# Kernel tuning notes

Hardware: AMD Instinct MI355X
Metric: run time of the kernel (lower is better)

Reference implementation:

```python
import jax, jax.numpy as jnp
import numpy as np

DIM, H, D = 2048, 16, 128
D_C, D_CQ, D_ROPE = 512, 1536, 64
B, T = 2, 2048


def _rope(t, cos, sin):
    # t: [..., T, D_ROPE]; cos/sin: [T, D_ROPE//2] broadcast over leading dims
    h = D_ROPE // 2
    t1, t2 = t[..., :h], t[..., h:]
    return jnp.concatenate([t1 * cos - t2 * sin, t2 * cos + t1 * sin], axis=-1)


def setup_inputs() -> dict:
    key = jax.random.key(0)
    ks = jax.random.split(key, 10)
    init = lambda k, shp, fan: (jax.random.normal(k, shp, jnp.float32) / np.sqrt(fan).astype(np.float32))
    x = jax.random.normal(ks[0], (B, T, DIM), jnp.float32)
    # RoPE tables for d_rope//2 = 32 rotary channels
    inv_freq = 1.0 / (10000.0 ** (np.arange(0, D_ROPE // 2, dtype=np.float32) / (D_ROPE // 2)))
    ang = np.arange(T, dtype=np.float32)[:, None] * inv_freq[None, :]
    cos = jnp.asarray(np.cos(ang), jnp.float32)
    sin = jnp.asarray(np.sin(ang), jnp.float32)
    return {
        "x": x,
        "cos": cos,
        "sin": sin,
        "w_kv": init(ks[1], (DIM, D_C), DIM),          # kv_compress
        "w_kdec": init(ks[2], (D_C, H * D), D_C),       # k_decompress
        "w_vdec": init(ks[3], (D_C, H * D), D_C),       # v_decompress
        "w_qc": init(ks[4], (DIM, D_CQ), DIM),          # q_compress
        "w_qdec": init(ks[5], (D_CQ, H * D), D_CQ),     # q_decompress
        "w_krope": init(ks[6], (DIM, D_ROPE), DIM),     # k_rope_proj
        "w_qrope": init(ks[7], (DIM, D_ROPE), DIM),     # q_rope_proj
        "w_o": init(ks[8], (H * D, DIM), H * D),        # wo
    }


def reference(x, cos, sin, w_kv, w_kdec, w_vdec, w_qc, w_qdec, w_krope, w_qrope, w_o):
    Bx, Tx, _ = x.shape
    # latent compress -> decompress
    c_kv = x @ w_kv                                       # [B,T,d_c]
    k = (c_kv @ w_kdec).reshape(Bx, Tx, H, D).transpose(0, 2, 1, 3)  # [B,H,T,D]
    v = (c_kv @ w_vdec).reshape(Bx, Tx, H, D).transpose(0, 2, 1, 3)
    c_q = x @ w_qc
    q = (c_q @ w_qdec).reshape(Bx, Tx, H, D).transpose(0, 2, 1, 3)
    # RoPE branch: head-shared projections, rotated then broadcast across heads
    k_rope = _rope(x @ w_krope, cos, sin)                 # [B,T,d_rope]
    q_rope = _rope(x @ w_qrope, cos, sin)
    rope_dim = min(D_ROPE, D)
    qr = jnp.broadcast_to(q_rope[:, None, :, :rope_dim], (Bx, H, Tx, rope_dim))
    kr = jnp.broadcast_to(k_rope[:, None, :, :rope_dim], (Bx, H, Tx, rope_dim))
    q = jnp.concatenate([q[..., :-rope_dim], qr], axis=-1)
    k = jnp.concatenate([k[..., :-rope_dim], kr], axis=-1)
    # causal SDPA, scale = 1/sqrt(head_dim)
    scores = jnp.einsum("bhtd,bhsd->bhts", q, k) / np.float32(np.sqrt(D))
    causal = jnp.tril(jnp.ones((Tx, Tx), dtype=bool))
    scores = jnp.where(causal, scores, jnp.float32(-1e30))
    attn = jax.nn.softmax(scores, axis=-1)
    out = jnp.einsum("bhts,bhsd->bhtd", attn, v)
    out = out.transpose(0, 2, 1, 3).reshape(Bx, Tx, H * D)
    return out @ w_o
```

## Files before the change

### kernel.cpp

```cpp
#include <hip/hip_runtime.h>
#include <stdint.h>
#include <math.h>

#define B_    2
#define T_    2048
#define DIM_  2048
#define H_    16
#define DC_   512
#define DCQ_  1536
#define NROWS (B_*T_)

typedef unsigned short u16;
typedef __attribute__((ext_vector_type(8))) __bf16 bf16x8;
typedef __attribute__((ext_vector_type(4))) float  f32x4;
typedef __attribute__((ext_vector_type(8))) unsigned short u16x8;
typedef __attribute__((ext_vector_type(4))) float  f4v;

__device__ __forceinline__ u16 f2bf(float f){
  unsigned u = __float_as_uint(f);
  u += 0x7FFFu + ((u >> 16) & 1u);
  return (u16)(u >> 16);
}
__device__ __forceinline__ float bf2f(u16 h){ return __uint_as_float(((unsigned)h) << 16); }

__device__ __forceinline__ unsigned cvt_pk_bf16(float lo, float hi){
  unsigned r;
  asm("v_cvt_pk_bf16_f32 %0, %1, %2" : "=v"(r) : "v"(lo), "v"(hi));
  return r;
}

__device__ __forceinline__ void gld_lds16(const void* g, void* l){
  auto gp = reinterpret_cast<__attribute__((address_space(1))) unsigned int*>(
      reinterpret_cast<uintptr_t>(g));
  auto lp = reinterpret_cast<__attribute__((address_space(3))) unsigned int*>(
      reinterpret_cast<uintptr_t>(l));
  __builtin_amdgcn_global_load_lds(gp, lp, 16, 0, 0);
}

__device__ __forceinline__ f32x4 mfma16(bf16x8 a, bf16x8 b, f32x4 c){
  return __builtin_amdgcn_mfma_f32_16x16x32_bf16(a, b, c, 0, 0, 0);
}

__device__ __forceinline__ void vmwait0(){ asm volatile("s_waitcnt vmcnt(0)" ::: "memory"); }
__device__ __forceinline__ void vmwait8(){ asm volatile("s_waitcnt vmcnt(8)" ::: "memory"); }
__device__ __forceinline__ void barr(){ asm volatile("s_barrier" ::: "memory"); }

__global__ void k_detect(const u16* cosr, int* flag, int* ticket){
  if (threadIdx.x == 0) *flag = (cosr[0] == (u16)0x3F80u) ? 1 : 0;
  if (threadIdx.x < 128) ticket[threadIdx.x] = 0;
}

struct TDesc { const void* src; u16* dst; int srcStride, dstStride, cblk, nbx, blk0; };
struct TPack { TDesc d[8]; };
#define CONVBLK 8192

__global__ void k_prep(const void* __restrict__ xsrc, u16* __restrict__ x_bf,
                       TPack p, const int* flag){
  __shared__ u16 tile[64][72];
  const int bid = blockIdx.x;
  const int tid = threadIdx.x;
  const int f = *flag;
  if (bid < CONVBLK){
    if (f) return;
    int id = bid * 256 + tid;
    f4v v = reinterpret_cast<const f4v*>(xsrc)[id];
    unsigned lo = (unsigned)f2bf(v.x) | ((unsigned)f2bf(v.y) << 16);
    unsigned hi = (unsigned)f2bf(v.z) | ((unsigned)f2bf(v.w) << 16);
    reinterpret_cast<uint2*>(x_bf)[id] = make_uint2(lo, hi);
    return;
  }
  const int tb = bid - CONVBLK;
  int i = 0;
  #pragma unroll
  for (int k = 1; k < 8; ++k) if (tb >= p.d[k].blk0) i = k;
  const void* src = p.d[i].src;
  u16* dst = p.d[i].dst;
  const int srcStride = p.d[i].srcStride, dstStride = p.d[i].dstStride;
  const int rel = tb - p.d[i].blk0;
  const int bx = rel % p.d[i].nbx, by = rel / p.d[i].nbx;
  const int r0 = by << 6, c0 = bx * p.d[i].cblk;
  #pragma unroll
  for (int it = 0; it < 2; ++it){
    int task = (it << 8) + tid;
    int r = task >> 3, c8 = (task & 7) << 3;
    if (f){
      const u16* pp = (const u16*)src + (size_t)(r0 + r) * srcStride + c0 + c8;
      u16x8 v = *reinterpret_cast<const u16x8*>(pp);
      #pragma unroll
      for (int j = 0; j < 8; ++j) tile[r][c8 + j] = v[j];
    } else {
      const float* pp = (const float*)src + (size_t)(r0 + r) * srcStride + c0 + c8;
      f4v a = reinterpret_cast<const f4v*>(pp)[0];
      f4v b = reinterpret_cast<const f4v*>(pp)[1];
      tile[r][c8+0]=f2bf(a.x); tile[r][c8+1]=f2bf(a.y); tile[r][c8+2]=f2bf(a.z); tile[r][c8+3]=f2bf(a.w);
      tile[r][c8+4]=f2bf(b.x); tile[r][c8+5]=f2bf(b.y); tile[r][c8+6]=f2bf(b.z); tile[r][c8+7]=f2bf(b.w);
    }
  }
  __syncthreads();
  #pragma unroll
  for (int it = 0; it < 2; ++it){
    int task = (it << 8) + tid;
    int rr = task >> 3, cc8 = (task & 7) << 3;
    u16x8 v;
    #pragma unroll
    for (int j = 0; j < 8; ++j) v[j] = tile[cc8 + j][rr];
    *reinterpret_cast<u16x8*>(dst + (size_t)((bx << 6) + rr) * dstStride + r0 + cc8) = v;
  }
}

__global__ __launch_bounds__(256, 2) void k_gemm(
    const u16* __restrict__ A0, int lda0, const u16* __restrict__ Bt0, int K0,
    u16* __restrict__ C0, int ldc0, float os0,
    const u16* __restrict__ A1, int lda1, const u16* __restrict__ Bt1, int K1,
    u16* __restrict__ C1, int ldc1, float os1,
    int ysplit, int swz, void* outp, const int* flag,
    const u16* __restrict__ alt0, const u16* __restrict__ alt1,
    u16* __restrict__ vt0, u16* __restrict__ vt1){
  __shared__ alignas(16) u16 lds[32768];
  const int tid = threadIdx.x;
  const int wid = tid >> 6, lane = tid & 63;
  const int wr = wid >> 1, wc = wid & 1;
  const int l16 = lane & 15, g = lane >> 4;
  int lin = blockIdx.y * 32 + blockIdx.x;
  if (swz){
    const int q8 = (gridDim.x * gridDim.y) >> 3;
    lin = (lin & 7) * q8 + (lin >> 3);
  }
  const int m0 = (lin & 31) << 7;
  int nt = lin >> 5;
  const u16 *A, *Bt, *alt; u16 *C, *vtp; int lda, K, ldc; float oscale;
  if (nt < ysplit){ A = A0; lda = lda0; Bt = Bt0; K = K0; C = C0; ldc = ldc0; oscale = os0; alt = alt0; vtp = vt0; }
  else { nt -= ysplit; A = A1; lda = lda1; Bt = Bt1; K = K1; C = C1; ldc = ldc1; oscale = os1; alt = alt1; vtp = vt1; }
  const int f = flag ? *flag : 1;
  if (alt && f) A = alt;
  const int n0 = nt << 7;
  const size_t Kz = (size_t)K;
  const int nkt = K >> 6;

  auto STAGE = [&](int kt, int bufn){
    const int kb = kt << 6;
    #pragma unroll
    for (int q = 0; q < 8; ++q){
      const int ht = q >> 2;
      const int cq = ((q & 3) << 8) + tid;
      const int Lb = cq << 4;
      const int row = Lb >> 7;
      const int colb = (Lb & 127) ^ ((row & 7) << 4);
      const u16* src = ht ? (Bt + (size_t)(n0 + row) * Kz + kb + (colb >> 1))
                          : (A  + (size_t)(m0 + row) * lda + kb + (colb >> 1));
      gld_lds16(src, &lds[bufn * 16384 + ht * 8192 + (cq << 3)]);
    }
  };

  f32x4 acc[4][4] = {};

  STAGE(0, 0);
  int buf = 0;

  for (int kt = 0; kt < nkt; ++kt){
    if (kt + 1 < nkt){ STAGE(kt + 1, buf ^ 1); vmwait8(); }
    else vmwait0();
    barr();
    bf16x8 af[2][4], bfr[2][4];
    #pragma unroll
    for (int ks = 0; ks < 2; ++ks){
      #pragma unroll
      for (int mi = 0; mi < 4; ++mi){
        int row = (wr << 6) + (mi << 4) + l16;
        int cb = ((ks << 6) + (g << 4)) ^ ((row & 7) << 4);
        af[ks][mi] = *reinterpret_cast<const bf16x8*>(&lds[buf * 16384 + (((row << 7) + cb) >> 1)]);
      }
      #pragma unroll
      for (int ni = 0; ni < 4; ++ni){
        int row = (wc << 6) + (ni << 4) + l16;
        int cb = ((ks << 6) + (g << 4)) ^ ((row & 7) << 4);
        bfr[ks][ni] = *reinterpret_cast<const bf16x8*>(&lds[buf * 16384 + 8192 + (((row << 7) + cb) >> 1)]);
      }
    }
    __builtin_amdgcn_s_setprio(1);
    #pragma unroll
    for (int ks = 0; ks < 2; ++ks)
      #pragma unroll
      for (int mi = 0; mi < 4; ++mi)
        #pragma unroll
        for (int ni = 0; ni < 4; ++ni)
          acc[mi][ni] = mfma16(af[ks][mi], bfr[ks][ni], acc[mi][ni]);
    __builtin_amdgcn_s_setprio(0);
    barr();
    buf ^= 1;
  }

  const int r4 = g << 2;
  #pragma unroll
  for (int mi = 0; mi < 4; ++mi){
    int row = m0 + (wr << 6) + (mi << 4) + r4;
    #pragma unroll
    for (int ni = 0; ni < 4; ++ni){
      int col = n0 + (wc << 6) + (ni << 4) + l16;
      if (vtp && col >= 1024){
        int hd = col - 1024;
        u16* dst = vtp + (((size_t)(((row >> 11) << 4) + (hd >> 7)) << 7) + (hd & 127)) * (size_t)T_ + (row & (T_ - 1));
        union { u16 u[4]; uint2 v; } pk;
        #pragma unroll
        for (int j = 0; j < 4; ++j) pk.u[j] = f2bf(acc[mi][ni][j] * oscale);
        *reinterpret_cast<uint2*>(dst) = pk.v;
        continue;
      }
      #pragma unroll
      for (int j = 0; j < 4; ++j){
        float v = acc[mi][ni][j] * oscale;
        if (outp){
          if (f) ((u16*)outp)[(size_t)(row + j) * ldc + col] = f2bf(v);
          else   ((float*)outp)[(size_t)(row + j) * ldc + col] = v;
        } else {
          C[(size_t)(row + j) * ldc + col] = f2bf(v);
        }
      }
    }
  }
}

__global__ void k_rope(const u16* __restrict__ xc, const void* __restrict__ cosp,
                       const void* __restrict__ sinp, const int* flag,
                       u16* __restrict__ krope, u16* __restrict__ qrope){
  int id = blockIdx.x * 256 + threadIdx.x;
  int row = id >> 7, c = id & 127;
  int t = row & (T_ - 1);
  int d = c & 63, i = d & 31;
  float cs, sn;
  if (*flag){ cs = bf2f(((const u16*)cosp)[t * 32 + i]); sn = bf2f(((const u16*)sinp)[t * 32 + i]); }
  else      { cs = ((const float*)cosp)[t * 32 + i];     sn = ((const float*)sinp)[t * 32 + i]; }
  int base = c & 64;
  float t1 = bf2f(xc[(size_t)row * 2304 + 2048 + base + i]);
  float t2 = bf2f(xc[(size_t)row * 2304 + 2048 + base + 32 + i]);
  float v = (d < 32) ? (t1 * cs - t2 * sn) : (t2 * cs + t1 * sn);
  if (c >= 64) v *= 0.12753139626374414f;
  ((c < 64) ? krope : qrope)[(size_t)row * 64 + d] = f2bf(v);
}

__global__ __launch_bounds__(512, 2) void k_attn(const u16* __restrict__ qP,
                                                 const u16* __restrict__ kvP,
                                                 const u16* __restrict__ vT,
                                                 const u16* __restrict__ krope,
                                                 const u16* __restrict__ qrope,
                                                 u16* __restrict__ aout,
                                                 int* __restrict__ ticket){
  __shared__ alignas(16) u16 smem[32768];
  const int tid = threadIdx.x, wid = tid >> 6, lane = tid & 63;
  const int l16 = lane & 15, g = lane >> 4;
  const int lk = g << 3, r4 = g << 2;
  const int sw8 = (l16 & 7) << 3;
  const int xcd = blockIdx.x & 7;

  while (true){
    if (tid == 0) *(int*)&smem[0] = atomicAdd(&ticket[xcd << 4], 1);
    __syncthreads();
    const int it = *(const int*)&smem[0];
    __syncthreads();
    if (it >= 64) break;
    const int qt = 15 - (it >> 2);
    const int bh = (xcd << 2) + (it & 3), b = bh >> 4, h = bh & 15;
    const int q0 = qt << 7;
    const size_t bT = (size_t)b * T_;
    const u16* kvPb = kvP + bT * 1024 + (h << 6);
    const u16* krb  = krope + bT * 64;
    const u16* vTb  = vT + (size_t)bh * 128 * T_;
    const int qlo = q0 + (wid << 4);
    const int qhi = qlo + 15;
    const int nkv = (qt << 1) + 2;

    auto STAGE = [&](int buf, int k0){
      const int base = buf << 14;
      #pragma unroll
      for (int r = 0; r < 4; ++r){
        int c = (r << 9) + tid;
        const u16* src;
        if (r < 2){
          int row = c >> 4, cc = c & 15;
          int ccx = (cc & 8) | ((cc & 7) ^ (row & 7));
          int col0 = ccx << 3;
          src = (col0 < 64) ? (kvPb + (size_t)(k0 + row) * 1024 + col0)
                            : (krb  + (size_t)(k0 + row) * 64 + (col0 - 64));
        } else {
          int cv = c - 1024;
          int row = cv >> 3, cc = cv & 7;
          int ccx = cc ^ (row & 7);
          src = vTb + (size_t)row * T_ + k0 + (ccx << 3);
        }
        gld_lds16(src, &smem[base + (c << 3)]);
      }
    };

    bf16x8 qf[4];
    {
      size_t grow = bT + qlo + l16;
      #pragma unroll
      for (int ks = 0; ks < 4; ++ks){
        int d = (ks << 5) + lk;
        const u16* src = (ks < 2) ? (qP + grow * 1024 + (h << 6) + d)
                                  : (qrope + grow * 64 + (d - 64));
        qf[ks] = *reinterpret_cast<const bf16x8*>(src);
      }
    }
    f32x4 o[8] = {};
    float m = -3e38f, l = 0.f;

    STAGE(0, 0);
    __syncthreads();
    int cur = 0;

    for (int kv = 0; kv < nkv; ++kv){
      const int k0 = kv << 6;
      if (kv + 1 < nkv) STAGE(cur ^ 1, (kv + 1) << 6);
      if (k0 <= qhi){
        const int kb = cur << 14;
        f32x4 s[4] = {};
        __builtin_amdgcn_s_setprio(1);
        #pragma unroll
        for (int ks = 0; ks < 4; ++ks){
          int colsw = ((ks << 5) + lk) ^ sw8;
          #pragma unroll
          for (int n = 0; n < 4; ++n){
            bf16x8 kf = *reinterpret_cast<const bf16x8*>(&smem[kb + ((n << 4) + l16) * 128 + colsw]);
            s[n] = mfma16(kf, qf[ks], s[n]);
          }
        }
        __builtin_amdgcn_s_setprio(0);
        if (k0 + 63 > qlo){
          const int tq = qlo + l16;
          #pragma unroll
          for (int n = 0; n < 4; ++n)
            #pragma unroll
            for (int j = 0; j < 4; ++j)
              s[n][j] = (k0 + (n << 4) + r4 + j <= tq) ? s[n][j] : -3e38f;
        }
        float mx;
        {
          float a0 = fmaxf(fmaxf(s[0][0], s[0][1]), fmaxf(s[0][2], s[0][3]));
          float a1 = fmaxf(fmaxf(s[1][0], s[1][1]), fmaxf(s[1][2], s[1][3]));
          float a2 = fmaxf(fmaxf(s[2][0], s[2][1]), fmaxf(s[2][2], s[2][3]));
          float a3 = fmaxf(fmaxf(s[3][0], s[3][1]), fmaxf(s[3][2], s[3][3]));
          mx = fmaxf(fmaxf(a0, a1), fmaxf(a2, a3));
          mx = fmaxf(mx, __shfl_xor(mx, 16));
          mx = fmaxf(mx, __shfl_xor(mx, 32));
        }
        if (__ballot(mx > m + 8.f)){
          float mnew = fmaxf(m, mx);
          float alpha = exp2f(m - mnew);
          m = mnew; l *= alpha;
          #pragma unroll
          for (int j = 0; j < 4; ++j){
            float av = __shfl(alpha, r4 + j);
            #pragma unroll
            for (int db = 0; db < 8; ++db) o[db][j] *= av;
          }
        }
        unsigned w[4][2];
        float rs = 0.f;
        #pragma unroll
        for (int n = 0; n < 4; ++n)
          #pragma unroll
          for (int jh = 0; jh < 2; ++jh){
            float p0 = exp2f(s[n][2*jh]     - m);
            float p1 = exp2f(s[n][2*jh + 1] - m);
            rs += p0 + p1;
            w[n][jh] = cvt_pk_bf16(p0, p1);
          }
        rs += __shfl_xor(rs, 16);
        rs += __shfl_xor(rs, 32);
        l += rs;
        const int srcA = l16 + ((g & 1) << 5);
        const int srcB = srcA + 16;
        const bool hi = (g >= 2);
        bf16x8 pa[2];
        #pragma unroll
        for (int ks2 = 0; ks2 < 2; ++ks2){
          unsigned a0 = __shfl((int)w[2*ks2][0],     srcA);
          unsigned b0 = __shfl((int)w[2*ks2 + 1][0], srcA);
          unsigned a1 = __shfl((int)w[2*ks2][1],     srcA);
          unsigned b1 = __shfl((int)w[2*ks2 + 1][1], srcA);
          unsigned a2 = __shfl((int)w[2*ks2][0],     srcB);
          unsigned b2 = __shfl((int)w[2*ks2 + 1][0], srcB);
          unsigned a3 = __shfl((int)w[2*ks2][1],     srcB);
          unsigned b3 = __shfl((int)w[2*ks2 + 1][1], srcB);
          union { unsigned u[4]; bf16x8 v; } pk;
          pk.u[0] = hi ? b0 : a0;
          pk.u[1] = hi ? b1 : a1;
          pk.u[2] = hi ? b2 : a2;
          pk.u[3] = hi ? b3 : a3;
          pa[ks2] = pk.v;
        }
        __builtin_amdgcn_s_setprio(1);
        #pragma unroll
        for (int ks2 = 0; ks2 < 2; ++ks2){
          int colsw = ((ks2 << 5) + lk) ^ sw8;
          #pragma unroll
          for (int db = 0; db < 8; ++db){
            bf16x8 vb = *reinterpret_cast<const bf16x8*>(&smem[(cur << 14) + 8192 + ((db << 4) + l16) * 64 + colsw]);
            o[db] = mfma16(pa[ks2], vb, o[db]);
          }
        }
        __builtin_amdgcn_s_setprio(0);
      }
      __syncthreads();
      cur ^= 1;
    }
    #pragma unroll
    for (int j = 0; j < 4; ++j){
      float lv = __shfl(l, r4 + j);
      float rinv = 1.f / lv;
      const int tq = qlo + r4 + j;
      u16* dst = aout + (bT + tq) * 2048 + (h << 7) + l16;
      #pragma unroll
      for (int db = 0; db < 8; ++db)
        dst[db << 4] = f2bf(o[db][j] * rinv);
    }
  }
}

extern "C" void kernel_launch(void* const* d_in, const int* in_sizes, int n_in,
                              void* d_out, int out_size, void* d_ws, size_t ws_size,
                              hipStream_t stream){
  const void* x       = d_in[0];
  const void* cosp    = d_in[1];
  const void* sinp    = d_in[2];
  const void* w_kv    = d_in[3];
  const void* w_kdec  = d_in[4];
  const void* w_vdec  = d_in[5];
  const void* w_qc    = d_in[6];
  const void* w_qdec  = d_in[7];
  const void* w_krope = d_in[8];
  const void* w_qrope = d_in[9];
  const void* w_o     = d_in[10];

  char* ws = (char*)d_ws;
  size_t off = 0;
  auto alloc = [&](size_t bytes){ void* p = ws + off; off += (bytes + 255) & ~(size_t)255; return p; };
  int* flag     = (int*)alloc(256);
  int* ticket   = (int*)alloc(1024);
  u16* x_bf     = (u16*)alloc((size_t)NROWS * DIM_ * 2);
  u16* w_c1T    = (u16*)alloc((size_t)2304 * DIM_ * 2);
  u16* w_kvdT   = (u16*)alloc((size_t)3072 * DC_ * 2);
  u16* w_qdPT   = (u16*)alloc((size_t)1024 * DCQ_ * 2);
  u16* w_oT     = (u16*)alloc((size_t)DIM_ * DIM_ * 2);
  u16* xc       = (u16*)alloc((size_t)NROWS * 2304 * 2);
  u16* qP       = (u16*)alloc((size_t)NROWS * 1024 * 2);
  u16* kvP      = (u16*)alloc((size_t)NROWS * 1024 * 2);
  u16* krope    = (u16*)alloc((size_t)NROWS * 64 * 2);
  u16* qrope    = (u16*)alloc((size_t)NROWS * 64 * 2);
  u16* vT       = (u16*)alloc((size_t)32 * 128 * T_ * 2);
  u16* aout     = (u16*)alloc((size_t)NROWS * DIM_ * 2);
  (void)in_sizes; (void)n_in; (void)out_size; (void)ws_size;

  const float SC2 = 0.12753139626374414f;

  hipLaunchKernelGGL(k_detect, dim3(1), dim3(128), 0, stream, (const u16*)cosp, flag, ticket);

  TPack tp;
  tp.d[0] = { w_kv,    w_c1T,                        512,  2048, 64,  8,  0    };
  tp.d[1] = { w_qc,    w_c1T + (size_t)512 * 2048,   1536, 2048, 64,  24, 256  };
  tp.d[2] = { w_krope, w_c1T + (size_t)2048 * 2048,  64,   2048, 64,  1,  1024 };
  tp.d[3] = { w_qrope, w_c1T + (size_t)2112 * 2048,  64,   2048, 64,  1,  1056 };
  tp.d[4] = { w_kdec,  w_kvdT,                       2048, 512,  128, 16, 1088 };
  tp.d[5] = { w_vdec,  w_kvdT + (size_t)1024 * 512,  2048, 512,  64,  32, 1216 };
  tp.d[6] = { w_qdec,  w_qdPT,                       2048, 1536, 128, 16, 1472 };
  tp.d[7] = { w_o,     w_oT,                         2048, 2048, 64,  32, 1856 };
  hipLaunchKernelGGL(k_prep, dim3(CONVBLK + 2880), dim3(256), 0, stream, x, x_bf, tp, flag);

  hipLaunchKernelGGL(k_gemm, dim3(32, 18), dim3(256), 0, stream,
                     x_bf, DIM_, w_c1T, DIM_, xc, 2304, 1.0f,
                     x_bf, DIM_, w_c1T, DIM_, xc, 2304, 1.0f,
                     18, 1, (void*)nullptr, (const int*)flag,
                     (const u16*)x, (const u16*)x,
                     (u16*)nullptr, (u16*)nullptr);
  hipLaunchKernelGGL(k_gemm, dim3(32, 32), dim3(256), 0, stream,
                     xc + 512, 2304, w_qdPT, DCQ_, qP, 1024, SC2,
                     xc, 2304, w_kvdT, DC_, kvP, 1024, 1.0f,
                     8, 0, (void*)nullptr, (const int*)nullptr,
                     (const u16*)nullptr, (const u16*)nullptr,
                     (u16*)nullptr, vT);
  hipLaunchKernelGGL(k_rope, dim3(2048), dim3(256), 0, stream,
                     xc, cosp, sinp, flag, krope, qrope);
  hipLaunchKernelGGL(k_attn, dim3(256), dim3(512), 0, stream,
                     qP, kvP, vT, krope, qrope, aout, ticket);
  hipLaunchKernelGGL(k_gemm, dim3(32, 16), dim3(256), 0, stream,
                     aout, DIM_, w_oT, DIM_, (u16*)nullptr, DIM_, 1.0f,
                     aout, DIM_, w_oT, DIM_, (u16*)nullptr, DIM_, 1.0f,
                     16, 1, d_out, (const int*)flag,
                     (const u16*)nullptr, (const u16*)nullptr,
                     (u16*)nullptr, (u16*)nullptr);
}
```

Before: 247.4 us.

## Fuse RoPE into first projection GEMM epilogue and drop padding tile

The RoPE rotation and q-scaling move into the epilogue of the compress GEMM. The tile holding the k/q rope projection columns rotates its accumulators in registers, pairing column d with column d±32 within the same warp, and writes krope and qrope directly. This removes the separate k_rope kernel launch and its reread of xc. The grid also shrinks from 18 to 17 column tiles, since the last tile was unused padding. The cost is extra parameters and a branch in the shared GEMM kernel, plus scattered 2-byte epilogue stores for that tile.

```diff
diff --git a/kernel.cpp b/kernel.cpp
--- a/kernel.cpp
+++ b/kernel.cpp
@@ -115,7 +115,9 @@
     u16* __restrict__ C1, int ldc1, float os1,
     int ysplit, int swz, void* outp, const int* flag,
     const u16* __restrict__ alt0, const u16* __restrict__ alt1,
-    u16* __restrict__ vt0, u16* __restrict__ vt1){
+    u16* __restrict__ vt0, u16* __restrict__ vt1,
+    const void* __restrict__ cosp, const void* __restrict__ sinp,
+    u16* __restrict__ ropeK, u16* __restrict__ ropeQ){
   __shared__ alignas(16) u16 lds[32768];
   const int tid = threadIdx.x;
   const int wid = tid >> 6, lane = tid & 63;
@@ -191,6 +193,33 @@
   }
 
   const int r4 = g << 2;
+
+  if (ropeK && nt == 16){
+    const int dbase = l16;
+    #pragma unroll
+    for (int mi = 0; mi < 4; ++mi){
+      int row = m0 + (wr << 6) + (mi << 4) + r4;
+      #pragma unroll
+      for (int ni = 0; ni < 4; ++ni){
+        const int d = (ni << 4) + dbase;
+        const int i = d & 31;
+        #pragma unroll
+        for (int j = 0; j < 4; ++j){
+          int t = (row + j) & (T_ - 1);
+          float cs, sn;
+          if (f){ cs = bf2f(((const u16*)cosp)[t * 32 + i]); sn = bf2f(((const u16*)sinp)[t * 32 + i]); }
+          else  { cs = ((const float*)cosp)[t * 32 + i];     sn = ((const float*)sinp)[t * 32 + i]; }
+          float own = acc[mi][ni][j];
+          float par = acc[mi][ni ^ 2][j];
+          float v = (d < 32) ? (own * cs - par * sn) : (own * cs + par * sn);
+          if (wc) v *= 0.12753139626374414f;
+          (wc ? ropeQ : ropeK)[(size_t)(row + j) * 64 + d] = f2bf(v);
+        }
+      }
+    }
+    return;
+  }
+
   #pragma unroll
   for (int mi = 0; mi < 4; ++mi){
     int row = m0 + (wr << 6) + (mi << 4) + r4;
@@ -218,24 +247,6 @@
       }
     }
   }
-}
-
-__global__ void k_rope(const u16* __restrict__ xc, const void* __restrict__ cosp,
-                       const void* __restrict__ sinp, const int* flag,
-                       u16* __restrict__ krope, u16* __restrict__ qrope){
-  int id = blockIdx.x * 256 + threadIdx.x;
-  int row = id >> 7, c = id & 127;
-  int t = row & (T_ - 1);
-  int d = c & 63, i = d & 31;
-  float cs, sn;
-  if (*flag){ cs = bf2f(((const u16*)cosp)[t * 32 + i]); sn = bf2f(((const u16*)sinp)[t * 32 + i]); }
-  else      { cs = ((const float*)cosp)[t * 32 + i];     sn = ((const float*)sinp)[t * 32 + i]; }
-  int base = c & 64;
-  float t1 = bf2f(xc[(size_t)row * 2304 + 2048 + base + i]);
-  float t2 = bf2f(xc[(size_t)row * 2304 + 2048 + base + 32 + i]);
-  float v = (d < 32) ? (t1 * cs - t2 * sn) : (t2 * cs + t1 * sn);
-  if (c >= 64) v *= 0.12753139626374414f;
-  ((c < 64) ? krope : qrope)[(size_t)row * 64 + d] = f2bf(v);
 }
 
 __global__ __launch_bounds__(512, 2) void k_attn(const u16* __restrict__ qP,
@@ -467,20 +478,21 @@
   tp.d[7] = { w_o,     w_oT,                         2048, 2048, 64,  32, 1856 };
   hipLaunchKernelGGL(k_prep, dim3(CONVBLK + 2880), dim3(256), 0, stream, x, x_bf, tp, flag);
 
-  hipLaunchKernelGGL(k_gemm, dim3(32, 18), dim3(256), 0, stream,
+  hipLaunchKernelGGL(k_gemm, dim3(32, 17), dim3(256), 0, stream,
                      x_bf, DIM_, w_c1T, DIM_, xc, 2304, 1.0f,
                      x_bf, DIM_, w_c1T, DIM_, xc, 2304, 1.0f,
-                     18, 1, (void*)nullptr, (const int*)flag,
+                     17, 1, (void*)nullptr, (const int*)flag,
                      (const u16*)x, (const u16*)x,
-                     (u16*)nullptr, (u16*)nullptr);
+                     (u16*)nullptr, (u16*)nullptr,
+                     cosp, sinp, krope, qrope);
   hipLaunchKernelGGL(k_gemm, dim3(32, 32), dim3(256), 0, stream,
                      xc + 512, 2304, w_qdPT, DCQ_, qP, 1024, SC2,
                      xc, 2304, w_kvdT, DC_, kvP, 1024, 1.0f,
                      8, 0, (void*)nullptr, (const int*)nullptr,
                      (const u16*)nullptr, (const u16*)nullptr,
-                     (u16*)nullptr, vT);
-  hipLaunchKernelGGL(k_rope, dim3(2048), dim3(256), 0, stream,
-                     xc, cosp, sinp, flag, krope, qrope);
+                     (u16*)nullptr, vT,
+                     (const void*)nullptr, (const void*)nullptr,
+                     (u16*)nullptr, (u16*)nullptr);
   hipLaunchKernelGGL(k_attn, dim3(256), dim3(512), 0, stream,
                      qP, kvP, vT, krope, qrope, aout, ticket);
   hipLaunchKernelGGL(k_gemm, dim3(32, 16), dim3(256), 0, stream,
@@ -488,5 +500,7 @@
                      aout, DIM_, w_oT, DIM_, (u16*)nullptr, DIM_, 1.0f,
                      16, 1, d_out, (const int*)flag,
                      (const u16*)nullptr, (const u16*)nullptr,
+                     (u16*)nullptr, (u16*)nullptr,
+                     (const void*)nullptr, (const void*)nullptr,
                      (u16*)nullptr, (u16*)nullptr);
 }
```

Result: slower. 252.7 us (+2.2%).
